# Optimization experiments

Measured on AMD Instinct MI355X. Metric: run time of the kernel, lower is better.

Reference implementation:

```python
import jax, jax.numpy as jnp
import numpy as np

EMBED_DIM = 1024
NUM_HEADS = 16
HEAD_DIM = EMBED_DIM // NUM_HEADS
B, T = 4, 2048


def setup_inputs() -> dict:
    key = jax.random.key(0)
    ks = jax.random.split(key, 5)
    s = 0.02
    return {
        "x": jax.random.normal(ks[0], (B, T, EMBED_DIM), dtype=jnp.float32),
        "qkv_w": jax.random.normal(ks[1], (3 * EMBED_DIM, EMBED_DIM), dtype=jnp.float32) * s,
        "qkv_b": jax.random.normal(ks[2], (3 * EMBED_DIM,), dtype=jnp.float32) * s,
        "out_w": jax.random.normal(ks[3], (EMBED_DIM, EMBED_DIM), dtype=jnp.float32) * s,
        "out_b": jax.random.normal(ks[4], (EMBED_DIM,), dtype=jnp.float32) * s,
    }


def reference(x, qkv_w, qkv_b, out_w, out_b):
    b, t, c = x.shape
    h, d = NUM_HEADS, HEAD_DIM
    # qkv projection: Linear uses y = x @ W^T + b
    qkv = jnp.einsum("btc,fc->btf", x, qkv_w) + qkv_b  # [B,T,3C]
    q, k, v = jnp.split(qkv, 3, axis=-1)
    # [B, H, T, D]
    q = q.reshape(b, t, h, d).transpose(0, 2, 1, 3)
    k = k.reshape(b, t, h, d).transpose(0, 2, 1, 3)
    v = v.reshape(b, t, h, d).transpose(0, 2, 1, 3)
    scores = jnp.einsum("bhqd,bhkd->bhqk", q, k) / jnp.sqrt(jnp.float32(d))
    causal = jnp.tril(jnp.ones((t, t), dtype=bool))
    scores = jnp.where(causal, scores, -jnp.inf)
    attn = jax.nn.softmax(scores, axis=-1)
    o = jnp.einsum("bhqk,bhkd->bhqd", attn, v)
    o = o.transpose(0, 2, 1, 3).reshape(b, t, c)
    return jnp.einsum("btc,fc->btf", o, out_w) + out_b
```

## Files before the change

### kernel.cpp

```cpp
#include <hip/hip_runtime.h>
#include <hip/hip_bf16.h>
#include <math.h>

#define SEQ   2048
#define NTOK  8192
#define EMB   1024
#define QKVF  3072

typedef __bf16 bf16;
typedef __bf16 bf16x8 __attribute__((ext_vector_type(8)));
typedef __bf16 bf16x4 __attribute__((ext_vector_type(4)));
typedef float  f32x4  __attribute__((ext_vector_type(4)));

__device__ __forceinline__ void gload_lds16(const bf16* g, bf16* l) {
    __builtin_amdgcn_global_load_lds(
        (const __attribute__((address_space(1))) unsigned int*)g,
        (__attribute__((address_space(3))) unsigned int*)l,
        16, 0, 0);
}

__global__ __launch_bounds__(256) void cvt_f32_bf16(const float* __restrict__ in,
                                                    bf16* __restrict__ out, int n) {
    int i = (blockIdx.x * 256 + threadIdx.x) * 4;
    if (i >= n) return;
    float4 f = *reinterpret_cast<const float4*>(in + i);
    bf16x4 o;
    o[0] = (bf16)f.x; o[1] = (bf16)f.y; o[2] = (bf16)f.z; o[3] = (bf16)f.w;
    *reinterpret_cast<bf16x4*>(out + i) = o;
}

template <bool BF16OUT>
__global__ __launch_bounds__(256) void gemm_bt(const bf16* __restrict__ A,
                                               const bf16* __restrict__ Bm,
                                               const float* __restrict__ bias,
                                               void* __restrict__ out,
                                               int M, int N, int K) {
    __shared__ bf16 As[128 * 64];
    __shared__ bf16 Bs[128 * 64];

    const int nbx = N >> 7;
    const int nwg = nbx * (M >> 7);
    const int q8  = nwg >> 3;
    const int swz = (blockIdx.x & 7) * q8 + (blockIdx.x >> 3);
    const int bx  = swz % nbx;
    const int by  = swz / nbx;

    const int tid  = threadIdx.x;
    const int lane = tid & 63;
    const int wv   = tid >> 6;
    const int wr   = wv >> 1, wc = wv & 1;
    const int lr   = lane & 15, hi = lane >> 4;
    const size_t brow = (size_t)by * 128;
    const size_t bcol = (size_t)bx * 128;

    const f32x4 fzero = {0.f, 0.f, 0.f, 0.f};
    f32x4 acc[4][4];
#pragma unroll
    for (int m = 0; m < 4; ++m)
#pragma unroll
        for (int n = 0; n < 4; ++n) acc[m][n] = fzero;

    const int r8 = tid >> 3;
    const int c8 = tid & 7;

    for (int kt = 0; kt < K; kt += 64) {
#pragma unroll
        for (int i = 0; i < 4; ++i) {
            const int row = i * 32 + r8;
            const int lin = i * 256 + tid;
            gload_lds16(A  + (brow + row) * (size_t)K + kt + c8 * 8, &As[lin * 8]);
            gload_lds16(Bm + (bcol + row) * (size_t)K + kt + c8 * 8, &Bs[lin * 8]);
        }
        __syncthreads();
#pragma unroll
        for (int kk = 0; kk < 2; ++kk) {
            bf16x8 af[4], bfr[4];
#pragma unroll
            for (int m = 0; m < 4; ++m)
                af[m] = *reinterpret_cast<const bf16x8*>(
                    &As[(wr * 64 + m * 16 + lr) * 64 + kk * 32 + hi * 8]);
#pragma unroll
            for (int n = 0; n < 4; ++n)
                bfr[n] = *reinterpret_cast<const bf16x8*>(
                    &Bs[(wc * 64 + n * 16 + lr) * 64 + kk * 32 + hi * 8]);
#pragma unroll
            for (int m = 0; m < 4; ++m)
#pragma unroll
                for (int n = 0; n < 4; ++n)
                    acc[m][n] = __builtin_amdgcn_mfma_f32_16x16x32_bf16(
                        af[m], bfr[n], acc[m][n], 0, 0, 0);
        }
        __syncthreads();
    }

#pragma unroll
    for (int m = 0; m < 4; ++m)
#pragma unroll
        for (int n = 0; n < 4; ++n)
#pragma unroll
            for (int r = 0; r < 4; ++r) {
                const size_t row = brow + wr * 64 + m * 16 + hi * 4 + r;
                const size_t col = bcol + wc * 64 + n * 16 + lr;
                const float v = acc[m][n][r] + bias[col];
                if (BF16OUT)
                    ((bf16*)out)[row * (size_t)N + col] = (bf16)v;
                else
                    ((float*)out)[row * (size_t)N + col] = v;
            }
}

__global__ __launch_bounds__(256) void attn_kernel(const bf16* __restrict__ qkv,
                                                   bf16* __restrict__ o) {
    const int bid = blockIdx.x;
    const int qt  = 15 - (bid >> 6);
    const int bh  = bid & 63;
    const int h   = bh & 15;
    const int b   = bh >> 4;
    const int qbase = qt * 128;

    const int tid  = threadIdx.x;
    const int wv   = tid >> 6;
    const int lane = tid & 63;
    const int lr   = lane & 15, hi = lane >> 4;

    __shared__ bf16 Ks[64 * 64];
    __shared__ bf16 Vt[64 * 64];
    __shared__ bf16 Pl[4 * 32 * 64];

    char* Ksb = (char*)Ks;
    char* Vtb = (char*)Vt;
    char* Pb  = (char*)(Pl + wv * 2048);

    const size_t tokbase = (size_t)b * SEQ;

    bf16x8 aq[2][2];
#pragma unroll
    for (int qf = 0; qf < 2; ++qf) {
        const bf16* qg = qkv + (tokbase + qbase + wv * 32 + qf * 16 + lr) * (size_t)QKVF
                         + h * 64;
#pragma unroll
        for (int kk = 0; kk < 2; ++kk)
            aq[qf][kk] = *reinterpret_cast<const bf16x8*>(qg + kk * 32 + hi * 8);
    }

    const f32x4 fzero = {0.f, 0.f, 0.f, 0.f};
    f32x4 oacc[2][4];
#pragma unroll
    for (int qf = 0; qf < 2; ++qf)
#pragma unroll
        for (int n = 0; n < 4; ++n) oacc[qf][n] = fzero;
    float m_r[2] = {-__builtin_inff(), -__builtin_inff()};
    float l_r[2] = {0.f, 0.f};

    const int nkv = qt * 2 + 2;
    const float SC = 0.125f * 1.44269504f;

    const int vk0 = tid >> 3;
    const int vc  = tid & 7;

    for (int kt = 0; kt < nkv; ++kt) {
        const size_t kvrow = tokbase + (size_t)kt * 64;
        __syncthreads();

#pragma unroll
        for (int j = 0; j < 2; ++j) {
            const int kr = wv * 16 + j * 8 + (lane >> 3);
            const int cg = (lane & 7) ^ ((lane >> 3) & 7);
            gload_lds16(qkv + (kvrow + kr) * (size_t)QKVF + EMB + h * 64 + cg * 8,
                        &Ks[(wv * 16 + j * 8) * 64 + lane * 8]);
        }

        {
            bf16x8 v0 = *reinterpret_cast<const bf16x8*>(
                qkv + (kvrow + vk0) * (size_t)QKVF + 2 * EMB + h * 64 + vc * 8);
            bf16x8 v1 = *reinterpret_cast<const bf16x8*>(
                qkv + (kvrow + vk0 + 32) * (size_t)QKVF + 2 * EMB + h * 64 + vc * 8);
#pragma unroll
            for (int jj = 0; jj < 8; ++jj) {
                const int d = vc * 8 + jj;
                char* row = Vtb + d * 128;
                *(bf16*)(row + ((vk0 * 2) ^ (vc << 4)))        = v0[jj];
                *(bf16*)(row + (((vk0 + 32) * 2) ^ (vc << 4))) = v1[jj];
            }
        }
        __syncthreads();

        f32x4 s[2][4];
#pragma unroll
        for (int qf = 0; qf < 2; ++qf)
#pragma unroll
            for (int ktile = 0; ktile < 4; ++ktile) s[qf][ktile] = fzero;
#pragma unroll
        for (int ktile = 0; ktile < 4; ++ktile)
#pragma unroll
            for (int kk = 0; kk < 2; ++kk) {
                const int kr = ktile * 16 + lr;
                bf16x8 ak = *reinterpret_cast<const bf16x8*>(
                    Ksb + kr * 128 + ((kk * 64 + hi * 16) ^ ((kr & 7) << 4)));
#pragma unroll
                for (int qf = 0; qf < 2; ++qf)
                    s[qf][ktile] = __builtin_amdgcn_mfma_f32_16x16x32_bf16(
                        ak, aq[qf][kk], s[qf][ktile], 0, 0, 0);
            }

#pragma unroll
        for (int qf = 0; qf < 2; ++qf) {
            const int qglob = qbase + wv * 32 + qf * 16 + lr;
#pragma unroll
            for (int ktile = 0; ktile < 4; ++ktile) {
                const int kg0 = kt * 64 + ktile * 16 + hi * 4;
#pragma unroll
                for (int r = 0; r < 4; ++r) {
                    const float sv = s[qf][ktile][r] * SC;
                    s[qf][ktile][r] = (kg0 + r <= qglob) ? sv : -__builtin_inff();
                }
            }
        }

#pragma unroll
        for (int qf = 0; qf < 2; ++qf) {
            float tm = s[qf][0][0];
#pragma unroll
            for (int ktile = 0; ktile < 4; ++ktile)
#pragma unroll
                for (int r = 0; r < 4; ++r) tm = fmaxf(tm, s[qf][ktile][r]);
            tm = fmaxf(tm, __shfl_xor(tm, 16));
            tm = fmaxf(tm, __shfl_xor(tm, 32));

            const float mn = fmaxf(m_r[qf], tm);
            const float sc = __builtin_amdgcn_exp2f(m_r[qf] - mn);
            m_r[qf] = mn;

            float ts = 0.f;
#pragma unroll
            for (int ktile = 0; ktile < 4; ++ktile)
#pragma unroll
                for (int r = 0; r < 4; ++r) {
                    const float p = __builtin_amdgcn_exp2f(s[qf][ktile][r] - mn);
                    s[qf][ktile][r] = p;
                    ts += p;
                }
            ts += __shfl_xor(ts, 16);
            ts += __shfl_xor(ts, 32);
            l_r[qf] = l_r[qf] * sc + ts;

            float scb[4];
#pragma unroll
            for (int r = 0; r < 4; ++r) scb[r] = __shfl(sc, hi * 4 + r);
#pragma unroll
            for (int n = 0; n < 4; ++n)
#pragma unroll
                for (int r = 0; r < 4; ++r) oacc[qf][n][r] *= scb[r];

            const int q = qf * 16 + lr;
#pragma unroll
            for (int ktile = 0; ktile < 4; ++ktile) {
                bf16x4 p4;
#pragma unroll
                for (int r = 0; r < 4; ++r) p4[r] = (bf16)s[qf][ktile][r];
                *(bf16x4*)(Pb + q * 128 + ((ktile * 32 + hi * 8) ^ ((q & 7) << 4))) = p4;
            }
        }

#pragma unroll
        for (int kk = 0; kk < 2; ++kk) {
            bf16x8 ap[2];
#pragma unroll
            for (int qf = 0; qf < 2; ++qf) {
                const int q = qf * 16 + lr;
                ap[qf] = *reinterpret_cast<const bf16x8*>(
                    Pb + q * 128 + ((kk * 64 + hi * 16) ^ ((q & 7) << 4)));
            }
#pragma unroll
            for (int n = 0; n < 4; ++n) {
                const int d = n * 16 + lr;
                bf16x8 bv = *reinterpret_cast<const bf16x8*>(
                    Vtb + d * 128 + ((kk * 64 + hi * 16) ^ (((d >> 3) & 7) << 4)));
#pragma unroll
                for (int qf = 0; qf < 2; ++qf)
                    oacc[qf][n] = __builtin_amdgcn_mfma_f32_16x16x32_bf16(
                        ap[qf], bv, oacc[qf][n], 0, 0, 0);
            }
        }
    }

#pragma unroll
    for (int qf = 0; qf < 2; ++qf) {
        const float linv = 1.f / l_r[qf];
        float li[4];
#pragma unroll
        for (int r = 0; r < 4; ++r) li[r] = __shfl(linv, hi * 4 + r);
        bf16* og = o + (tokbase + qbase + wv * 32 + qf * 16) * (size_t)EMB + h * 64;
#pragma unroll
        for (int n = 0; n < 4; ++n)
#pragma unroll
            for (int r = 0; r < 4; ++r)
                og[(hi * 4 + r) * (size_t)EMB + n * 16 + lr] =
                    (bf16)(oacc[qf][n][r] * li[r]);
    }
}

extern "C" void kernel_launch(void* const* d_in, const int* in_sizes, int n_in,
                              void* d_out, int out_size, void* d_ws, size_t ws_size,
                              hipStream_t stream) {
    const float* x     = (const float*)d_in[0];
    const float* qkv_w = (const float*)d_in[1];
    const float* qkv_b = (const float*)d_in[2];
    const float* out_w = (const float*)d_in[3];
    const float* out_b = (const float*)d_in[4];
    float* out = (float*)d_out;

    char* ws = (char*)d_ws;
    bf16* x_bf    = (bf16*)(ws);
    bf16* qkvw_bf = (bf16*)(ws + 16777216);
    bf16* outw_bf = (bf16*)(ws + 23068672);
    bf16* qkv_bf  = (bf16*)(ws + 25165824);
    bf16* o_bf    = (bf16*)(ws + 75497472);

    cvt_f32_bf16<<<8192, 256, 0, stream>>>(x,     x_bf,    NTOK * EMB);
    cvt_f32_bf16<<<3072, 256, 0, stream>>>(qkv_w, qkvw_bf, QKVF * EMB);
    cvt_f32_bf16<<<1024, 256, 0, stream>>>(out_w, outw_bf, EMB * EMB);

    gemm_bt<true><<<(QKVF / 128) * (NTOK / 128), 256, 0, stream>>>(
        x_bf, qkvw_bf, qkv_b, qkv_bf, NTOK, QKVF, EMB);

    attn_kernel<<<4 * 16 * (SEQ / 128), 256, 0, stream>>>(qkv_bf, o_bf);

    gemm_bt<false><<<(EMB / 128) * (NTOK / 128), 256, 0, stream>>>(
        o_bf, outw_bf, out_b, out, NTOK, EMB, EMB);
}
```

Measured before the change: 297.7 us.

## Replace GEMM with 8-wave double-buffered, LDS-swizzled, ping-pong pipelined kernel

```diff
diff --git a/kernel.cpp b/kernel.cpp
--- a/kernel.cpp
+++ b/kernel.cpp
@@ -29,84 +29,153 @@
     *reinterpret_cast<bf16x4*>(out + i) = o;
 }
 
-template <bool BF16OUT>
-__global__ __launch_bounds__(256) void gemm_bt(const bf16* __restrict__ A,
-                                               const bf16* __restrict__ Bm,
-                                               const float* __restrict__ bias,
-                                               void* __restrict__ out,
-                                               int M, int N, int K) {
-    __shared__ bf16 As[128 * 64];
-    __shared__ bf16 Bs[128 * 64];
-
-    const int nbx = N >> 7;
-    const int nwg = nbx * (M >> 7);
+template <int NF, bool BF16OUT>
+__global__ __launch_bounds__(512, 2) void gemm_bt8(const bf16* __restrict__ A,
+                                                   const bf16* __restrict__ Bm,
+                                                   const float* __restrict__ bias,
+                                                   void* __restrict__ out,
+                                                   int M, int N, int K) {
+    constexpr int NBR = NF / 2;
+    constexpr int WN  = NBR + 2;
+    __shared__ bf16 As[2][256 * 64];
+    __shared__ bf16 Bs[2][2][NF * 64 * 32];
+
+    const int nbx = N / (NF * 64);
+    const int nwg = nbx * (M >> 8);
     const int q8  = nwg >> 3;
-    const int swz = (blockIdx.x & 7) * q8 + (blockIdx.x >> 3);
+    const int swz = ((int)blockIdx.x & 7) * q8 + ((int)blockIdx.x >> 3);
     const int bx  = swz % nbx;
     const int by  = swz / nbx;
 
     const int tid  = threadIdx.x;
     const int lane = tid & 63;
-    const int wv   = tid >> 6;
-    const int wr   = wv >> 1, wc = wv & 1;
+    const int wid  = tid >> 6;
+    const int wr   = wid >> 2, wc = wid & 3;
     const int lr   = lane & 15, hi = lane >> 4;
-    const size_t brow = (size_t)by * 128;
-    const size_t bcol = (size_t)bx * 128;
+    const size_t brow = (size_t)by * 256;
+    const size_t bcol = (size_t)bx * (NF * 64);
 
     const f32x4 fzero = {0.f, 0.f, 0.f, 0.f};
-    f32x4 acc[4][4];
-#pragma unroll
-    for (int m = 0; m < 4; ++m)
-#pragma unroll
-        for (int n = 0; n < 4; ++n) acc[m][n] = fzero;
-
-    const int r8 = tid >> 3;
-    const int c8 = tid & 7;
-
-    for (int kt = 0; kt < K; kt += 64) {
-#pragma unroll
-        for (int i = 0; i < 4; ++i) {
-            const int row = i * 32 + r8;
-            const int lin = i * 256 + tid;
-            gload_lds16(A  + (brow + row) * (size_t)K + kt + c8 * 8, &As[lin * 8]);
-            gload_lds16(Bm + (bcol + row) * (size_t)K + kt + c8 * 8, &Bs[lin * 8]);
-        }
-        __syncthreads();
-#pragma unroll
-        for (int kk = 0; kk < 2; ++kk) {
-            bf16x8 af[4], bfr[4];
-#pragma unroll
-            for (int m = 0; m < 4; ++m)
-                af[m] = *reinterpret_cast<const bf16x8*>(
-                    &As[(wr * 64 + m * 16 + lr) * 64 + kk * 32 + hi * 8]);
-#pragma unroll
-            for (int n = 0; n < 4; ++n)
-                bfr[n] = *reinterpret_cast<const bf16x8*>(
-                    &Bs[(wc * 64 + n * 16 + lr) * 64 + kk * 32 + hi * 8]);
-#pragma unroll
-            for (int m = 0; m < 4; ++m)
-#pragma unroll
-                for (int n = 0; n < 4; ++n)
-                    acc[m][n] = __builtin_amdgcn_mfma_f32_16x16x32_bf16(
-                        af[m], bfr[n], acc[m][n], 0, 0, 0);
-        }
-        __syncthreads();
+    f32x4 acc[8][NF];
+#pragma unroll
+    for (int m = 0; m < 8; ++m)
+#pragma unroll
+        for (int n = 0; n < NF; ++n) acc[m][n] = fzero;
+
+#define STAGE_A_ROUND(b, kt, r) do {                                            \
+    const int row_ = (r) * 64 + (tid >> 3);                                     \
+    const int cg_  = (tid & 7) ^ (row_ & 7);                                    \
+    gload_lds16(A + (brow + row_) * (size_t)K + (size_t)(kt) * 64 + cg_ * 8,    \
+                &As[b][(r) * 4096 + tid * 8]);                                  \
+} while (0)
+#define STAGE_B_ROUND(b, kt, kkp, rr) do {                                      \
+    const int row_ = (rr) * 128 + (tid >> 2);                                   \
+    const int cg_  = (tid & 3) ^ (row_ & 3);                                    \
+    gload_lds16(Bm + (bcol + row_) * (size_t)K + (size_t)(kt) * 64 +            \
+                    (kkp) * 32 + cg_ * 8,                                       \
+                &Bs[b][kkp][(rr) * 4096 + tid * 8]);                            \
+} while (0)
+#define ISSUE_G1(b, kt) do { STAGE_A_ROUND(b, kt, 0); STAGE_A_ROUND(b, kt, 2);  \
+    for (int rr_ = 0; rr_ < NBR; ++rr_) STAGE_B_ROUND(b, kt, 0, rr_); } while (0)
+#define ISSUE_G2(b, kt) do {                                                    \
+    for (int rr_ = 0; rr_ < NBR; ++rr_) STAGE_B_ROUND(b, kt, 1, rr_); } while (0)
+#define ISSUE_G3(b, kt) do { STAGE_A_ROUND(b, kt, 1); STAGE_A_ROUND(b, kt, 3); } while (0)
+
+#define READ_A(b, mh, kk, dst) do {                                             \
+    _Pragma("unroll")                                                           \
+    for (int i_ = 0; i_ < 4; ++i_) {                                            \
+        const int row_ = wr * 128 + (mh) * 64 + i_ * 16 + lr;                   \
+        dst[i_] = *reinterpret_cast<const bf16x8*>(                             \
+            (const char*)&As[b][0] + row_ * 128 +                               \
+            (((kk) * 64 + hi * 16) ^ ((row_ & 7) << 4)));                       \
+    }                                                                           \
+} while (0)
+#define READ_B(b, kk, dst) do {                                                 \
+    _Pragma("unroll")                                                           \
+    for (int n_ = 0; n_ < NF; ++n_) {                                           \
+        const int row_ = wc * (NF * 16) + n_ * 16 + lr;                         \
+        dst[n_] = *reinterpret_cast<const bf16x8*>(                             \
+            (const char*)&Bs[b][kk][0] + row_ * 64 +                            \
+            ((hi * 16) ^ ((row_ & 3) << 4)));                                   \
+    }                                                                           \
+} while (0)
+#define DO_MFMA(mh, afr, bfr) do {                                              \
+    __builtin_amdgcn_s_setprio(1);                                              \
+    _Pragma("unroll")                                                           \
+    for (int i_ = 0; i_ < 4; ++i_)                                              \
+        _Pragma("unroll")                                                       \
+        for (int n_ = 0; n_ < NF; ++n_)                                         \
+            acc[(mh) * 4 + i_][n_] = __builtin_amdgcn_mfma_f32_16x16x32_bf16(   \
+                afr[i_], bfr[n_], acc[(mh) * 4 + i_][n_], 0, 0, 0);             \
+    __builtin_amdgcn_s_setprio(0);                                              \
+} while (0)
+
+    const int NT = K >> 6;
+
+    ISSUE_G1(0, 0);
+    ISSUE_G2(0, 0);
+    ISSUE_G3(0, 0);
+    asm volatile("s_waitcnt vmcnt(%0)" :: "i"(WN) : "memory");
+    __builtin_amdgcn_s_barrier();
+
+    bf16x8 af[4], bk0[NF], bk1[NF];
+
+    for (int kt = 0; kt < NT; ++kt) {
+        const int  b    = kt & 1;
+        const int  nb   = b ^ 1;
+        const bool last = (kt == NT - 1);
+
+        if (!last) ISSUE_G1(nb, kt + 1);
+        READ_A(b, 0, 0, af);
+        READ_B(b, 0, bk0);
+        if (last) asm volatile("s_waitcnt vmcnt(0)" ::: "memory");
+        else      asm volatile("s_waitcnt vmcnt(%0)" :: "i"(WN) : "memory");
+        __builtin_amdgcn_s_barrier();
+        DO_MFMA(0, af, bk0);
+        __builtin_amdgcn_s_barrier();
+
+        if (!last) ISSUE_G2(nb, kt + 1);
+        READ_A(b, 0, 1, af);
+        READ_B(b, 1, bk1);
+        __builtin_amdgcn_s_barrier();
+        DO_MFMA(0, af, bk1);
+        __builtin_amdgcn_s_barrier();
+
+        if (!last) ISSUE_G3(nb, kt + 1);
+        READ_A(b, 1, 1, af);
+        __builtin_amdgcn_s_barrier();
+        DO_MFMA(1, af, bk1);
+        __builtin_amdgcn_s_barrier();
+
+        READ_A(b, 1, 0, af);
+        if (!last) asm volatile("s_waitcnt vmcnt(%0)" :: "i"(WN) : "memory");
+        __builtin_amdgcn_s_barrier();
+        DO_MFMA(1, af, bk0);
+        __builtin_amdgcn_s_barrier();
     }
 
 #pragma unroll
-    for (int m = 0; m < 4; ++m)
-#pragma unroll
-        for (int n = 0; n < 4; ++n)
+    for (int mf = 0; mf < 8; ++mf)
+#pragma unroll
+        for (int n = 0; n < NF; ++n)
 #pragma unroll
             for (int r = 0; r < 4; ++r) {
-                const size_t row = brow + wr * 64 + m * 16 + hi * 4 + r;
-                const size_t col = bcol + wc * 64 + n * 16 + lr;
-                const float v = acc[m][n][r] + bias[col];
+                const size_t row = brow + wr * 128 + mf * 16 + hi * 4 + r;
+                const size_t col = bcol + wc * (NF * 16) + n * 16 + lr;
+                const float v = acc[mf][n][r] + bias[col];
                 if (BF16OUT)
                     ((bf16*)out)[row * (size_t)N + col] = (bf16)v;
                 else
                     ((float*)out)[row * (size_t)N + col] = v;
             }
+#undef STAGE_A_ROUND
+#undef STAGE_B_ROUND
+#undef ISSUE_G1
+#undef ISSUE_G2
+#undef ISSUE_G3
+#undef READ_A
+#undef READ_B
+#undef DO_MFMA
 }
 
 __global__ __launch_bounds__(256) void attn_kernel(const bf16* __restrict__ qkv,
@@ -321,11 +390,11 @@
     cvt_f32_bf16<<<3072, 256, 0, stream>>>(qkv_w, qkvw_bf, QKVF * EMB);
     cvt_f32_bf16<<<1024, 256, 0, stream>>>(out_w, outw_bf, EMB * EMB);
 
-    gemm_bt<true><<<(QKVF / 128) * (NTOK / 128), 256, 0, stream>>>(
+    gemm_bt8<4, true><<<(QKVF / 256) * (NTOK / 256), 512, 0, stream>>>(
         x_bf, qkvw_bf, qkv_b, qkv_bf, NTOK, QKVF, EMB);
 
     attn_kernel<<<4 * 16 * (SEQ / 128), 256, 0, stream>>>(qkv_bf, o_bf);
 
-    gemm_bt<false><<<(EMB / 128) * (NTOK / 128), 256, 0, stream>>>(
+    gemm_bt8<2, false><<<(EMB / 128) * (NTOK / 256), 512, 0, stream>>>(
         o_bf, outw_bf, out_b, out, NTOK, EMB, EMB);
 }
```

Measured after the change: 315.2 us. 1.06x slower.

## Double-buffer GEMM LDS tiles, fold softmax scale into Q weights, skip unneeded masking

Applied to the files above, without the earlier changes.

```diff
diff --git a/kernel.cpp b/kernel.cpp
--- a/kernel.cpp
+++ b/kernel.cpp
@@ -6,6 +6,7 @@
 #define NTOK  8192
 #define EMB   1024
 #define QKVF  3072
+#define QSCALE 0.18033688f
 
 typedef __bf16 bf16;
 typedef __bf16 bf16x8 __attribute__((ext_vector_type(8)));
@@ -29,19 +30,29 @@
     *reinterpret_cast<bf16x4*>(out + i) = o;
 }
 
+__global__ __launch_bounds__(256) void cvt_qkvw_bf16(const float* __restrict__ in,
+                                                     bf16* __restrict__ out) {
+    int i = (blockIdx.x * 256 + threadIdx.x) * 4;
+    float4 f = *reinterpret_cast<const float4*>(in + i);
+    const float s = (i < EMB * EMB) ? QSCALE : 1.f;
+    bf16x4 o;
+    o[0] = (bf16)(f.x * s); o[1] = (bf16)(f.y * s);
+    o[2] = (bf16)(f.z * s); o[3] = (bf16)(f.w * s);
+    *reinterpret_cast<bf16x4*>(out + i) = o;
+}
+
 template <bool BF16OUT>
 __global__ __launch_bounds__(256) void gemm_bt(const bf16* __restrict__ A,
                                                const bf16* __restrict__ Bm,
                                                const float* __restrict__ bias,
                                                void* __restrict__ out,
-                                               int M, int N, int K) {
-    __shared__ bf16 As[128 * 64];
-    __shared__ bf16 Bs[128 * 64];
+                                               int M, int N, int K, int scale_cols) {
+    __shared__ bf16 As[2][128 * 64];
+    __shared__ bf16 Bs[2][128 * 64];
 
     const int nbx = N >> 7;
-    const int nwg = nbx * (M >> 7);
-    const int q8  = nwg >> 3;
-    const int swz = (blockIdx.x & 7) * q8 + (blockIdx.x >> 3);
+    const int q8  = (nbx * (M >> 7)) >> 3;
+    const int swz = ((int)blockIdx.x & 7) * q8 + ((int)blockIdx.x >> 3);
     const int bx  = swz % nbx;
     const int by  = swz / nbx;
 
@@ -63,26 +74,36 @@
     const int r8 = tid >> 3;
     const int c8 = tid & 7;
 
-    for (int kt = 0; kt < K; kt += 64) {
-#pragma unroll
-        for (int i = 0; i < 4; ++i) {
-            const int row = i * 32 + r8;
-            const int lin = i * 256 + tid;
-            gload_lds16(A  + (brow + row) * (size_t)K + kt + c8 * 8, &As[lin * 8]);
-            gload_lds16(Bm + (bcol + row) * (size_t)K + kt + c8 * 8, &Bs[lin * 8]);
-        }
-        __syncthreads();
+#define STAGE(buf, kt) do {                                                     \
+    _Pragma("unroll")                                                           \
+    for (int i_ = 0; i_ < 4; ++i_) {                                            \
+        const int row_ = i_ * 32 + r8;                                          \
+        const int lin_ = i_ * 256 + tid;                                        \
+        gload_lds16(A  + (brow + row_) * (size_t)K + (size_t)(kt) * 64 + c8*8,  \
+                    &As[buf][lin_ * 8]);                                        \
+        gload_lds16(Bm + (bcol + row_) * (size_t)K + (size_t)(kt) * 64 + c8*8,  \
+                    &Bs[buf][lin_ * 8]);                                        \
+    }                                                                           \
+} while (0)
+
+    const int NT = K >> 6;
+    STAGE(0, 0);
+    __syncthreads();
+    int cur = 0;
+
+    for (int kt = 0; kt < NT; ++kt) {
+        if (kt + 1 < NT) STAGE(cur ^ 1, kt + 1);
 #pragma unroll
         for (int kk = 0; kk < 2; ++kk) {
             bf16x8 af[4], bfr[4];
 #pragma unroll
             for (int m = 0; m < 4; ++m)
                 af[m] = *reinterpret_cast<const bf16x8*>(
-                    &As[(wr * 64 + m * 16 + lr) * 64 + kk * 32 + hi * 8]);
+                    &As[cur][(wr * 64 + m * 16 + lr) * 64 + kk * 32 + hi * 8]);
 #pragma unroll
             for (int n = 0; n < 4; ++n)
                 bfr[n] = *reinterpret_cast<const bf16x8*>(
-                    &Bs[(wc * 64 + n * 16 + lr) * 64 + kk * 32 + hi * 8]);
+                    &Bs[cur][(wc * 64 + n * 16 + lr) * 64 + kk * 32 + hi * 8]);
 #pragma unroll
             for (int m = 0; m < 4; ++m)
 #pragma unroll
@@ -91,6 +112,7 @@
                         af[m], bfr[n], acc[m][n], 0, 0, 0);
         }
         __syncthreads();
+        cur ^= 1;
     }
 
 #pragma unroll
@@ -101,12 +123,14 @@
             for (int r = 0; r < 4; ++r) {
                 const size_t row = brow + wr * 64 + m * 16 + hi * 4 + r;
                 const size_t col = bcol + wc * 64 + n * 16 + lr;
-                const float v = acc[m][n][r] + bias[col];
+                const float bb = bias[col];
+                const float v = acc[m][n][r] + (((int)col < scale_cols) ? bb * QSCALE : bb);
                 if (BF16OUT)
                     ((bf16*)out)[row * (size_t)N + col] = (bf16)v;
                 else
                     ((float*)out)[row * (size_t)N + col] = v;
             }
+#undef STAGE
 }
 
 __global__ __launch_bounds__(256) void attn_kernel(const bf16* __restrict__ qkv,
@@ -153,7 +177,6 @@
     float l_r[2] = {0.f, 0.f};
 
     const int nkv = qt * 2 + 2;
-    const float SC = 0.125f * 1.44269504f;
 
     const int vk0 = tid >> 3;
     const int vc  = tid & 7;
@@ -205,25 +228,26 @@
 
 #pragma unroll
         for (int qf = 0; qf < 2; ++qf) {
-            const int qglob = qbase + wv * 32 + qf * 16 + lr;
-#pragma unroll
-            for (int ktile = 0; ktile < 4; ++ktile) {
-                const int kg0 = kt * 64 + ktile * 16 + hi * 4;
-#pragma unroll
-                for (int r = 0; r < 4; ++r) {
-                    const float sv = s[qf][ktile][r] * SC;
-                    s[qf][ktile][r] = (kg0 + r <= qglob) ? sv : -__builtin_inff();
+            if (kt * 64 + 63 > qbase + wv * 32 + qf * 16) {
+                const int qglob = qbase + wv * 32 + qf * 16 + lr;
+#pragma unroll
+                for (int ktile = 0; ktile < 4; ++ktile) {
+                    const int kg0 = kt * 64 + ktile * 16 + hi * 4;
+#pragma unroll
+                    for (int r = 0; r < 4; ++r)
+                        if (kg0 + r > qglob) s[qf][ktile][r] = -__builtin_inff();
                 }
             }
         }
 
 #pragma unroll
         for (int qf = 0; qf < 2; ++qf) {
-            float tm = s[qf][0][0];
+            float t4[4];
 #pragma unroll
             for (int ktile = 0; ktile < 4; ++ktile)
-#pragma unroll
-                for (int r = 0; r < 4; ++r) tm = fmaxf(tm, s[qf][ktile][r]);
+                t4[ktile] = fmaxf(fmaxf(s[qf][ktile][0], s[qf][ktile][1]),
+                                  fmaxf(s[qf][ktile][2], s[qf][ktile][3]));
+            float tm = fmaxf(fmaxf(t4[0], t4[1]), fmaxf(t4[2], t4[3]));
             tm = fmaxf(tm, __shfl_xor(tm, 16));
             tm = fmaxf(tm, __shfl_xor(tm, 32));
 
@@ -231,15 +255,18 @@
             const float sc = __builtin_amdgcn_exp2f(m_r[qf] - mn);
             m_r[qf] = mn;
 
-            float ts = 0.f;
-#pragma unroll
-            for (int ktile = 0; ktile < 4; ++ktile)
-#pragma unroll
-                for (int r = 0; r < 4; ++r) {
-                    const float p = __builtin_amdgcn_exp2f(s[qf][ktile][r] - mn);
-                    s[qf][ktile][r] = p;
-                    ts += p;
-                }
+            float s4[4];
+#pragma unroll
+            for (int ktile = 0; ktile < 4; ++ktile) {
+                float p0 = __builtin_amdgcn_exp2f(s[qf][ktile][0] - mn);
+                float p1 = __builtin_amdgcn_exp2f(s[qf][ktile][1] - mn);
+                float p2 = __builtin_amdgcn_exp2f(s[qf][ktile][2] - mn);
+                float p3 = __builtin_amdgcn_exp2f(s[qf][ktile][3] - mn);
+                s[qf][ktile][0] = p0; s[qf][ktile][1] = p1;
+                s[qf][ktile][2] = p2; s[qf][ktile][3] = p3;
+                s4[ktile] = (p0 + p1) + (p2 + p3);
+            }
+            float ts = (s4[0] + s4[1]) + (s4[2] + s4[3]);
             ts += __shfl_xor(ts, 16);
             ts += __shfl_xor(ts, 32);
             l_r[qf] = l_r[qf] * sc + ts;
@@ -318,14 +345,14 @@
     bf16* o_bf    = (bf16*)(ws + 75497472);
 
     cvt_f32_bf16<<<8192, 256, 0, stream>>>(x,     x_bf,    NTOK * EMB);
-    cvt_f32_bf16<<<3072, 256, 0, stream>>>(qkv_w, qkvw_bf, QKVF * EMB);
+    cvt_qkvw_bf16<<<3072, 256, 0, stream>>>(qkv_w, qkvw_bf);
     cvt_f32_bf16<<<1024, 256, 0, stream>>>(out_w, outw_bf, EMB * EMB);
 
     gemm_bt<true><<<(QKVF / 128) * (NTOK / 128), 256, 0, stream>>>(
-        x_bf, qkvw_bf, qkv_b, qkv_bf, NTOK, QKVF, EMB);
+        x_bf, qkvw_bf, qkv_b, qkv_bf, NTOK, QKVF, EMB, EMB);
 
     attn_kernel<<<4 * 16 * (SEQ / 128), 256, 0, stream>>>(qkv_bf, o_bf);
 
     gemm_bt<false><<<(EMB / 128) * (NTOK / 128), 256, 0, stream>>>(
-        o_bf, outw_bf, out_b, out, NTOK, EMB, EMB);
-}
+        o_bf, outw_bf, out_b, out, NTOK, EMB, EMB, 0);
+}
```

After: 299.1 us. No clear change (+0.5%).
